# Performance work log

Measured on AMD Instinct MI355X. Metric: run time of the kernel, lower is better.

Reference implementation:

```python
import jax, jax.numpy as jnp
import numpy as np

B, L, D, V = 32, 64, 512, 50257


def setup_inputs() -> dict:
    key = jax.random.key(0)
    ks = jax.random.split(key, 11)
    s = 0.02
    return {
        "input_ids": jax.random.randint(ks[0], (B, L), 0, V),
        "hidden": jax.random.normal(ks[1], (B, L, D), dtype=jnp.float32),
        "emb": jax.random.normal(ks[2], (V, D), dtype=jnp.float32) * s,
        "Wb": jax.random.normal(ks[3], (1, L), dtype=jnp.float32) * s,  # bridge Linear(L,1)
        "bb": jnp.zeros((1,), dtype=jnp.float32),
        "W_ih": jax.random.normal(ks[4], (3 * D, D), dtype=jnp.float32) * s,
        "b_ih": jnp.zeros((3 * D,), dtype=jnp.float32),
        "W_hh": jax.random.normal(ks[5], (3 * D, D), dtype=jnp.float32) * s,
        "b_hh": jnp.zeros((3 * D,), dtype=jnp.float32),
        "Wp": jax.random.normal(ks[6], (V, D), dtype=jnp.float32) * s,  # projection Linear(D,V)
        "bp": jnp.zeros((V,), dtype=jnp.float32),
    }


def reference(input_ids, hidden, emb, Wb, bb, W_ih, b_ih, W_hh, b_hh, Wp, bp):
    # Teacher forcing (prob=1). Each of the L-1 loop steps feeds prefix
    # input[:, :i+1] through the GRU but keeps only gru_output[0], which
    # depends only on the first token and the bridged init state -> all
    # steps produce the identical logits. Compute once, broadcast.
    x0 = jax.nn.relu(emb[input_ids[:, 0]])                 # [B, D] relu(embed(first token))
    h0 = jnp.einsum("bld,l->bd", hidden, Wb[0]) + bb[0]   # bridge over seq dim -> [B, D]
    # PyTorch GRU cell (gate order r, z, n)
    gx = x0 @ W_ih.T + b_ih                                # [B, 3D]
    gh = h0 @ W_hh.T + b_hh                                # [B, 3D]
    gxr, gxz, gxn = jnp.split(gx, 3, axis=-1)
    ghr, ghz, ghn = jnp.split(gh, 3, axis=-1)
    r = jax.nn.sigmoid(gxr + ghr)
    z = jax.nn.sigmoid(gxz + ghz)
    n = jnp.tanh(gxn + r * ghn)
    h1 = (1.0 - z) * n + z * h0                            # [B, D]
    logits = h1 @ Wp.T + bp                                # [B, V]
    out = jnp.broadcast_to(logits[:, None, :], (B, L - 1, V))  # [B, L-1, V]
    return out
```

## Files before the change

### kernel.cpp

```cpp
#include <hip/hip_runtime.h>
#include <math.h>

#define B_  32
#define L_  64
#define D_  512
#define V_  50257
#define LM1 63
#define OUTROW ((size_t)LM1 * V_)

__global__ __launch_bounds__(512) void prep_kernel(
    const int*   __restrict__ ids,
    const float* __restrict__ hidden,
    const float* __restrict__ emb,
    const float* __restrict__ Wb,
    const float* __restrict__ bb,
    const float* __restrict__ W_ih,
    const float* __restrict__ b_ih,
    const float* __restrict__ W_hh,
    const float* __restrict__ b_hh,
    float*       __restrict__ h1out)
{
    const int b = blockIdx.x;
    const int d = threadIdx.x;

    __shared__ __align__(16) float sx0[D_];
    __shared__ __align__(16) float sh0[D_];

    const int id0 = ids[b * L_];
    float x0 = emb[(size_t)id0 * D_ + d];
    x0 = x0 > 0.f ? x0 : 0.f;

    float h0 = bb[0];
    const float* hb = hidden + (size_t)b * L_ * D_ + d;
    #pragma unroll 8
    for (int l = 0; l < L_; ++l) {
        h0 += hb[(size_t)l * D_] * Wb[l];
    }

    sx0[d] = x0;
    sh0[d] = h0;
    __syncthreads();

    float ar = b_ih[d],        az = b_ih[D_ + d],        an = b_ih[2 * D_ + d];
    float br = b_hh[d],        bz = b_hh[D_ + d],        bn = b_hh[2 * D_ + d];

    const float4* wir = (const float4*)(W_ih + (size_t)d * D_);
    const float4* wiz = (const float4*)(W_ih + (size_t)(D_ + d) * D_);
    const float4* win = (const float4*)(W_ih + (size_t)(2 * D_ + d) * D_);
    const float4* whr = (const float4*)(W_hh + (size_t)d * D_);
    const float4* whz = (const float4*)(W_hh + (size_t)(D_ + d) * D_);
    const float4* whn = (const float4*)(W_hh + (size_t)(2 * D_ + d) * D_);
    const float4* x4  = (const float4*)sx0;
    const float4* h4  = (const float4*)sh0;

    #pragma unroll 4
    for (int k = 0; k < D_ / 4; ++k) {
        const float4 xv = x4[k];
        const float4 hv = h4[k];
        float4 w;
        w = wir[k]; ar += w.x * xv.x + w.y * xv.y + w.z * xv.z + w.w * xv.w;
        w = wiz[k]; az += w.x * xv.x + w.y * xv.y + w.z * xv.z + w.w * xv.w;
        w = win[k]; an += w.x * xv.x + w.y * xv.y + w.z * xv.z + w.w * xv.w;
        w = whr[k]; br += w.x * hv.x + w.y * hv.y + w.z * hv.z + w.w * hv.w;
        w = whz[k]; bz += w.x * hv.x + w.y * hv.y + w.z * hv.z + w.w * hv.w;
        w = whn[k]; bn += w.x * hv.x + w.y * hv.y + w.z * hv.z + w.w * hv.w;
    }

    const float r = 1.f / (1.f + expf(-(ar + br)));
    const float z = 1.f / (1.f + expf(-(az + bz)));
    const float n = tanhf(an + r * bn);
    const float h0v = sh0[d];
    const float h1 = (1.f - z) * n + z * h0v;

    h1out[b * D_ + d] = h1;
}

__global__ __launch_bounds__(256) void logits_kernel(
    const float* __restrict__ h1,
    const float* __restrict__ Wp,
    const float* __restrict__ bp,
    float*       __restrict__ out)
{
    const int v = blockIdx.x * 256 + threadIdx.x;
    if (v >= V_) return;

    float acc[B_];
    #pragma unroll
    for (int b = 0; b < B_; ++b) acc[b] = 0.f;

    const float4* wp4 = (const float4*)(Wp + (size_t)v * D_);
    const float4* h14 = (const float4*)h1;

    #pragma unroll 2
    for (int k = 0; k < D_ / 4; ++k) {
        const float4 w = wp4[k];
        #pragma unroll
        for (int b = 0; b < B_; ++b) {
            const float4 h = h14[b * (D_ / 4) + k];
            acc[b] += w.x * h.x + w.y * h.y + w.z * h.z + w.w * h.w;
        }
    }

    const float bias = bp[v];
    #pragma unroll
    for (int b = 0; b < B_; ++b) {
        out[(size_t)b * OUTROW + v] = acc[b] + bias;
    }
}

__global__ __launch_bounds__(256) void bcast_kernel(float* out)
{
    const int b  = blockIdx.z;
    const int l  = blockIdx.y + 1;
    const int v0 = blockIdx.x * 1024 + threadIdx.x;

    const float* src = out + (size_t)b * OUTROW;
    float*       dst = out + (size_t)b * OUTROW + (size_t)l * V_;

    #pragma unroll
    for (int i = 0; i < 4; ++i) {
        const int v = v0 + i * 256;
        if (v < V_) {
            __builtin_nontemporal_store(src[v], dst + v);
        }
    }
}

extern "C" void kernel_launch(void* const* d_in, const int* in_sizes, int n_in,
                              void* d_out, int out_size, void* d_ws, size_t ws_size,
                              hipStream_t stream) {
    const int*   ids    = (const int*)  d_in[0];
    const float* hidden = (const float*)d_in[1];
    const float* emb    = (const float*)d_in[2];
    const float* Wb     = (const float*)d_in[3];
    const float* bb     = (const float*)d_in[4];
    const float* W_ih   = (const float*)d_in[5];
    const float* b_ih   = (const float*)d_in[6];
    const float* W_hh   = (const float*)d_in[7];
    const float* b_hh   = (const float*)d_in[8];
    const float* Wp     = (const float*)d_in[9];
    const float* bp     = (const float*)d_in[10];

    float* out = (float*)d_out;
    float* h1  = (float*)d_ws;

    prep_kernel<<<B_, D_, 0, stream>>>(ids, hidden, emb, Wb, bb,
                                       W_ih, b_ih, W_hh, b_hh, h1);

    logits_kernel<<<(V_ + 255) / 256, 256, 0, stream>>>(h1, Wp, bp, out);

    bcast_kernel<<<dim3((V_ + 1023) / 1024, LM1 - 1, B_), 256, 0, stream>>>(out);
}
```

Before: 990.6 us.

## Fuse logits with broadcast and split GRU prep into parallel gate GEMM

Merges the logits computation and the 63-way broadcast into one kernel, so each block writes its logits straight to all sequence positions instead of writing once and re-reading. Split-K over 4 wave groups with a shared-memory reduction gives more parallelism per vocab tile. The GRU prep is split into three kernels (x0/h0, a batched gate GEMM over 48 blocks, and a combine step) so the weight reads are spread over more blocks than the original 32. This adds extra launches and workspace use, and falls back to the old prep kernel when the workspace is too small.

```diff
diff --git a/kernel.cpp b/kernel.cpp
--- a/kernel.cpp
+++ b/kernel.cpp
@@ -8,120 +8,235 @@
 #define LM1 63
 #define OUTROW ((size_t)LM1 * V_)
 
-__global__ __launch_bounds__(512) void prep_kernel(
+__global__ __launch_bounds__(512) void x0h0_kernel(
     const int*   __restrict__ ids,
     const float* __restrict__ hidden,
     const float* __restrict__ emb,
     const float* __restrict__ Wb,
     const float* __restrict__ bb,
-    const float* __restrict__ W_ih,
-    const float* __restrict__ b_ih,
-    const float* __restrict__ W_hh,
-    const float* __restrict__ b_hh,
-    float*       __restrict__ h1out)
+    float*       __restrict__ x0buf,
+    float*       __restrict__ h0buf)
 {
     const int b = blockIdx.x;
     const int d = threadIdx.x;
 
+    const int id0 = ids[b * L_];
+    float x0 = emb[(size_t)id0 * D_ + d];
+    x0buf[b * D_ + d] = x0 > 0.f ? x0 : 0.f;
+
+    float h0 = bb[0];
+    const float* hb = hidden + (size_t)b * L_ * D_ + d;
+    #pragma unroll 8
+    for (int l = 0; l < L_; ++l) h0 += hb[(size_t)l * D_] * Wb[l];
+    h0buf[b * D_ + d] = h0;
+}
+
+__global__ __launch_bounds__(256) void gates_kernel(
+    const float* __restrict__ x0,
+    const float* __restrict__ h0,
+    const float* __restrict__ W_ih,
+    const float* __restrict__ W_hh,
+    float*       __restrict__ gx,
+    float*       __restrict__ gh)
+{
+    const int blk = blockIdx.x;
+    const int R0  = blk * 64;
+    const int m   = R0 / (3 * D_);
+    const int r0  = R0 % (3 * D_);
+    const float* __restrict__ W  = m ? W_hh : W_ih;
+    const float* __restrict__ xh = m ? h0 : x0;
+    float* __restrict__ g        = m ? gh : gx;
+
+    const int t  = threadIdx.x;
+    const int rl = t & 63;
+    const int kc = __builtin_amdgcn_readfirstlane(t >> 6);
+
+    const float4* w4  = (const float4*)(W + (size_t)(r0 + rl) * D_) + kc * 32;
+    const float4* xh4 = (const float4*)xh + kc * 32;
+
+    float acc[B_];
+    #pragma unroll
+    for (int b = 0; b < B_; ++b) acc[b] = 0.f;
+
+    #pragma unroll 4
+    for (int kk = 0; kk < 32; ++kk) {
+        const float4 w = w4[kk];
+        #pragma unroll
+        for (int b = 0; b < B_; ++b) {
+            const float4 h = xh4[(size_t)b * (D_ / 4) + kk];
+            acc[b] += w.x * h.x + w.y * h.y + w.z * h.z + w.w * h.w;
+        }
+    }
+
+    __shared__ float red[4][B_][64];
+    #pragma unroll
+    for (int b = 0; b < B_; ++b) red[kc][b][rl] = acc[b];
+    __syncthreads();
+
+    const int r4 = t & 15, bpair = t >> 4;
+    #pragma unroll
+    for (int i = 0; i < 2; ++i) {
+        const int b = 2 * bpair + i;
+        float4 s = make_float4(0.f, 0.f, 0.f, 0.f);
+        #pragma unroll
+        for (int c = 0; c < 4; ++c) {
+            const float4 u = *(const float4*)&red[c][b][4 * r4];
+            s.x += u.x; s.y += u.y; s.z += u.z; s.w += u.w;
+        }
+        *(float4*)(g + (size_t)b * (3 * D_) + r0 + 4 * r4) = s;
+    }
+}
+
+__global__ __launch_bounds__(256) void combine_kernel(
+    const float* __restrict__ gx,
+    const float* __restrict__ gh,
+    const float* __restrict__ b_ih,
+    const float* __restrict__ b_hh,
+    const float* __restrict__ h0buf,
+    float*       __restrict__ h1)
+{
+    const int i = blockIdx.x * 256 + threadIdx.x;
+    const int b = i >> 9, d = i & (D_ - 1);
+    const size_t g0 = (size_t)b * (3 * D_);
+
+    const float gxr = gx[g0 + d]            + b_ih[d];
+    const float gxz = gx[g0 + D_ + d]       + b_ih[D_ + d];
+    const float gxn = gx[g0 + 2 * D_ + d]   + b_ih[2 * D_ + d];
+    const float ghr = gh[g0 + d]            + b_hh[d];
+    const float ghz = gh[g0 + D_ + d]       + b_hh[D_ + d];
+    const float ghn = gh[g0 + 2 * D_ + d]   + b_hh[2 * D_ + d];
+
+    const float r = 1.f / (1.f + expf(-(gxr + ghr)));
+    const float z = 1.f / (1.f + expf(-(gxz + ghz)));
+    const float n = tanhf(gxn + r * ghn);
+    h1[i] = (1.f - z) * n + z * h0buf[i];
+}
+
+__global__ __launch_bounds__(512) void prep_kernel(
+    const int* __restrict__ ids, const float* __restrict__ hidden,
+    const float* __restrict__ emb, const float* __restrict__ Wb,
+    const float* __restrict__ bb, const float* __restrict__ W_ih,
+    const float* __restrict__ b_ih, const float* __restrict__ W_hh,
+    const float* __restrict__ b_hh, float* __restrict__ h1out)
+{
+    const int b = blockIdx.x;
+    const int d = threadIdx.x;
     __shared__ __align__(16) float sx0[D_];
     __shared__ __align__(16) float sh0[D_];
 
     const int id0 = ids[b * L_];
     float x0 = emb[(size_t)id0 * D_ + d];
     x0 = x0 > 0.f ? x0 : 0.f;
-
     float h0 = bb[0];
     const float* hb = hidden + (size_t)b * L_ * D_ + d;
     #pragma unroll 8
-    for (int l = 0; l < L_; ++l) {
-        h0 += hb[(size_t)l * D_] * Wb[l];
-    }
-
-    sx0[d] = x0;
-    sh0[d] = h0;
-    __syncthreads();
-
-    float ar = b_ih[d],        az = b_ih[D_ + d],        an = b_ih[2 * D_ + d];
-    float br = b_hh[d],        bz = b_hh[D_ + d],        bn = b_hh[2 * D_ + d];
-
+    for (int l = 0; l < L_; ++l) h0 += hb[(size_t)l * D_] * Wb[l];
+    sx0[d] = x0; sh0[d] = h0;
+    __syncthreads();
+
+    float ar = b_ih[d], az = b_ih[D_ + d], an = b_ih[2 * D_ + d];
+    float br = b_hh[d], bz = b_hh[D_ + d], bn = b_hh[2 * D_ + d];
     const float4* wir = (const float4*)(W_ih + (size_t)d * D_);
     const float4* wiz = (const float4*)(W_ih + (size_t)(D_ + d) * D_);
     const float4* win = (const float4*)(W_ih + (size_t)(2 * D_ + d) * D_);
     const float4* whr = (const float4*)(W_hh + (size_t)d * D_);
     const float4* whz = (const float4*)(W_hh + (size_t)(D_ + d) * D_);
     const float4* whn = (const float4*)(W_hh + (size_t)(2 * D_ + d) * D_);
-    const float4* x4  = (const float4*)sx0;
-    const float4* h4  = (const float4*)sh0;
-
+    const float4* x4 = (const float4*)sx0;
+    const float4* h4 = (const float4*)sh0;
     #pragma unroll 4
     for (int k = 0; k < D_ / 4; ++k) {
-        const float4 xv = x4[k];
-        const float4 hv = h4[k];
-        float4 w;
-        w = wir[k]; ar += w.x * xv.x + w.y * xv.y + w.z * xv.z + w.w * xv.w;
-        w = wiz[k]; az += w.x * xv.x + w.y * xv.y + w.z * xv.z + w.w * xv.w;
-        w = win[k]; an += w.x * xv.x + w.y * xv.y + w.z * xv.z + w.w * xv.w;
-        w = whr[k]; br += w.x * hv.x + w.y * hv.y + w.z * hv.z + w.w * hv.w;
-        w = whz[k]; bz += w.x * hv.x + w.y * hv.y + w.z * hv.z + w.w * hv.w;
-        w = whn[k]; bn += w.x * hv.x + w.y * hv.y + w.z * hv.z + w.w * hv.w;
-    }
-
+        const float4 xv = x4[k]; const float4 hv = h4[k]; float4 w;
+        w = wir[k]; ar += w.x*xv.x + w.y*xv.y + w.z*xv.z + w.w*xv.w;
+        w = wiz[k]; az += w.x*xv.x + w.y*xv.y + w.z*xv.z + w.w*xv.w;
+        w = win[k]; an += w.x*xv.x + w.y*xv.y + w.z*xv.z + w.w*xv.w;
+        w = whr[k]; br += w.x*hv.x + w.y*hv.y + w.z*hv.z + w.w*hv.w;
+        w = whz[k]; bz += w.x*hv.x + w.y*hv.y + w.z*hv.z + w.w*hv.w;
+        w = whn[k]; bn += w.x*hv.x + w.y*hv.y + w.z*hv.z + w.w*hv.w;
+    }
     const float r = 1.f / (1.f + expf(-(ar + br)));
     const float z = 1.f / (1.f + expf(-(az + bz)));
     const float n = tanhf(an + r * bn);
-    const float h0v = sh0[d];
-    const float h1 = (1.f - z) * n + z * h0v;
-
-    h1out[b * D_ + d] = h1;
-}
-
-__global__ __launch_bounds__(256) void logits_kernel(
+    h1out[b * D_ + d] = (1.f - z) * n + z * sh0[d];
+}
+
+__global__ __launch_bounds__(256) void logits_bcast_kernel(
     const float* __restrict__ h1,
     const float* __restrict__ Wp,
     const float* __restrict__ bp,
     float*       __restrict__ out)
 {
-    const int v = blockIdx.x * 256 + threadIdx.x;
-    if (v >= V_) return;
+    const int t  = threadIdx.x;
+    const int v0 = blockIdx.x * 64;
+    const int vl = t & 63;
+    const int kc = __builtin_amdgcn_readfirstlane(t >> 6);
+
+    const int v    = v0 + vl;
+    const int vrow = v < V_ ? v : V_ - 1;
+
+    const float4* wp4 = (const float4*)(Wp + (size_t)vrow * D_) + kc * 32;
+    const float4* h4  = (const float4*)h1 + kc * 32;
 
     float acc[B_];
     #pragma unroll
     for (int b = 0; b < B_; ++b) acc[b] = 0.f;
 
-    const float4* wp4 = (const float4*)(Wp + (size_t)v * D_);
-    const float4* h14 = (const float4*)h1;
-
-    #pragma unroll 2
-    for (int k = 0; k < D_ / 4; ++k) {
-        const float4 w = wp4[k];
+    #pragma unroll 4
+    for (int kk = 0; kk < 32; ++kk) {
+        const float4 w = wp4[kk];
         #pragma unroll
         for (int b = 0; b < B_; ++b) {
-            const float4 h = h14[b * (D_ / 4) + k];
+            const float4 h = h4[(size_t)b * (D_ / 4) + kk];
             acc[b] += w.x * h.x + w.y * h.y + w.z * h.z + w.w * h.w;
         }
     }
 
-    const float bias = bp[v];
-    #pragma unroll
-    for (int b = 0; b < B_; ++b) {
-        out[(size_t)b * OUTROW + v] = acc[b] + bias;
-    }
-}
-
-__global__ __launch_bounds__(256) void bcast_kernel(float* out)
-{
-    const int b  = blockIdx.z;
-    const int l  = blockIdx.y + 1;
-    const int v0 = blockIdx.x * 1024 + threadIdx.x;
-
-    const float* src = out + (size_t)b * OUTROW;
-    float*       dst = out + (size_t)b * OUTROW + (size_t)l * V_;
-
-    #pragma unroll
-    for (int i = 0; i < 4; ++i) {
-        const int v = v0 + i * 256;
-        if (v < V_) {
-            __builtin_nontemporal_store(src[v], dst + v);
+    __shared__ float red[4][B_][64];
+    float* lg = (float*)red;
+
+    #pragma unroll
+    for (int b = 0; b < B_; ++b) red[kc][b][vl] = acc[b];
+    __syncthreads();
+
+    const int r4 = t & 15, bpair = t >> 4;
+    const int vv = v0 + 4 * r4;
+    float4 bias;
+    if (vv + 4 <= V_) bias = *(const float4*)(bp + vv);
+    else {
+        bias.x = (vv + 0 < V_) ? bp[vv + 0] : 0.f;
+        bias.y = (vv + 1 < V_) ? bp[vv + 1] : 0.f;
+        bias.z = (vv + 2 < V_) ? bp[vv + 2] : 0.f;
+        bias.w = (vv + 3 < V_) ? bp[vv + 3] : 0.f;
+    }
+    float4 s[2];
+    #pragma unroll
+    for (int i = 0; i < 2; ++i) {
+        const int b = 2 * bpair + i;
+        float4 a = make_float4(bias.x, bias.y, bias.z, bias.w);
+        #pragma unroll
+        for (int c = 0; c < 4; ++c) {
+            const float4 u = *(const float4*)&red[c][b][4 * r4];
+            a.x += u.x; a.y += u.y; a.z += u.z; a.w += u.w;
+        }
+        s[i] = a;
+    }
+    __syncthreads();
+    #pragma unroll
+    for (int i = 0; i < 2; ++i) {
+        const int b = 2 * bpair + i;
+        *(float4*)&lg[b * 64 + 4 * r4] = s[i];
+    }
+    __syncthreads();
+
+    const int w    = t >> 6;
+    const bool ok  = (v0 + vl) < V_;
+    if (ok) {
+        for (int b = 0; b < B_; ++b) {
+            const float val = lg[b * 64 + vl];
+            float* base = out + (size_t)b * OUTROW + v0 + vl;
+            for (int l = w; l < LM1; l += 4) {
+                __builtin_nontemporal_store(val, base + (size_t)l * V_);
+            }
         }
     }
 }
@@ -129,6 +244,8 @@
 extern "C" void kernel_launch(void* const* d_in, const int* in_sizes, int n_in,
                               void* d_out, int out_size, void* d_ws, size_t ws_size,
                               hipStream_t stream) {
+    (void)in_sizes; (void)n_in; (void)out_size;
+
     const int*   ids    = (const int*)  d_in[0];
     const float* hidden = (const float*)d_in[1];
     const float* emb    = (const float*)d_in[2];
@@ -142,12 +259,24 @@
     const float* bp     = (const float*)d_in[10];
 
     float* out = (float*)d_out;
-    float* h1  = (float*)d_ws;
-
-    prep_kernel<<<B_, D_, 0, stream>>>(ids, hidden, emb, Wb, bb,
-                                       W_ih, b_ih, W_hh, b_hh, h1);
-
-    logits_kernel<<<(V_ + 255) / 256, 256, 0, stream>>>(h1, Wp, bp, out);
-
-    bcast_kernel<<<dim3((V_ + 1023) / 1024, LM1 - 1, B_), 256, 0, stream>>>(out);
-}
+    float* ws  = (float*)d_ws;
+
+    const size_t need_bytes = (size_t)(16384 * 2 + 49152 * 2 + 16384) * 4;
+    float* h1;
+    if (ws_size >= need_bytes) {
+        float* x0b = ws;
+        float* h0b = ws + 16384;
+        float* gx  = ws + 32768;
+        float* gh  = ws + 81920;
+        h1         = ws + 131072;
+        x0h0_kernel<<<B_, D_, 0, stream>>>(ids, hidden, emb, Wb, bb, x0b, h0b);
+        gates_kernel<<<48, 256, 0, stream>>>(x0b, h0b, W_ih, W_hh, gx, gh);
+        combine_kernel<<<64, 256, 0, stream>>>(gx, gh, b_ih, b_hh, h0b, h1);
+    } else {
+        h1 = ws;
+        prep_kernel<<<B_, D_, 0, stream>>>(ids, hidden, emb, Wb, bb,
+                                           W_ih, b_ih, W_hh, b_hh, h1);
+    }
+
+    logits_bcast_kernel<<<(V_ + 63) / 64, 256, 0, stream>>>(h1, Wp, bp, out);
+}
```

New measurement: 846.3 us. -14.6%, faster.
